# Optimization experiments

Measured on AMD Instinct MI355X. Metric: run time of the kernel, lower is better.

## Reference

```python
import jax, jax.numpy as jnp
import numpy as np

B, S, D, H = 2, 2048, 1024, 16
HD = D // H  # head_dim = 64
SCALE = HD ** -0.5


def setup_inputs() -> dict:
    key = jax.random.key(0)
    ks = jax.random.split(key, 10)
    std = D ** -0.5
    return {
        "x": jax.random.normal(ks[0], (B, S, D), jnp.float32),
        "y": jax.random.normal(ks[1], (B, S, D), jnp.float32),
        "Wq": jax.random.normal(ks[2], (D, D), jnp.float32) * std,
        "bq": jnp.zeros((D,), jnp.float32),
        "Wk": jax.random.normal(ks[3], (D, D), jnp.float32) * std,
        "bk": jnp.zeros((D,), jnp.float32),
        "Wv": jax.random.normal(ks[4], (D, D), jnp.float32) * std,
        "bv": jnp.zeros((D,), jnp.float32),
        "Wo": jax.random.normal(ks[5], (D, D), jnp.float32) * std,
        "bo": jnp.zeros((D,), jnp.float32),
    }


def reference(x, y, Wq, bq, Wk, bk, Wv, bv, Wo, bo):
    # Linear projections (torch Linear: x @ W.T + b; here W stored as [in,out])
    q = x @ Wq + bq  # [B,S,D]
    k = y @ Wk + bk
    v = y @ Wv + bv
    # split heads -> [B,H,S,hd]
    q = q.reshape(B, S, H, HD).transpose(0, 2, 1, 3)
    k = k.reshape(B, S, H, HD).transpose(0, 2, 1, 3)
    v = v.reshape(B, S, H, HD).transpose(0, 2, 1, 3)
    scores = jnp.einsum("bhqd,bhkd->bhqk", q, k) * SCALE  # [B,H,S,S]
    causal = jnp.tril(jnp.ones((S, S), dtype=bool))  # keep lower triangle
    scores = jnp.where(causal[None, None], scores, -jnp.inf)
    attn = jax.nn.softmax(scores, axis=-1)
    out = jnp.einsum("bhqk,bhkd->bhqd", attn, v)  # [B,H,S,hd]
    out = out.transpose(0, 2, 1, 3).reshape(B, S, D)
    return out @ Wo + bo
```

## Files before the change

### kernel.cpp

```cpp
#include <hip/hip_runtime.h>
#include <hip/hip_bf16.h>


#define BDIM 2
#define SDIM 2048
#define DDIM 1024
#define HDIM 16
#define HD   64
#define MDIM (BDIM*SDIM)
#define C2 0.18033688011112042f

using short8  = __attribute__((ext_vector_type(8))) short;
using floatx4 = __attribute__((ext_vector_type(4))) float;

static __device__ __forceinline__ unsigned short f2bf(float x) {
    union { float f; unsigned int u; } c; c.f = x;
    unsigned int r = (c.u + 0x7fffu + ((c.u >> 16) & 1u)) >> 16;
    return (unsigned short)r;
}

static __device__ __forceinline__ unsigned int pack2bf(float a, float b) {
    union { float f; unsigned int u; } ua, ub;
    ua.f = a; ub.f = b;
    return __builtin_amdgcn_perm(ub.u + 0x8000u, ua.u + 0x8000u, 0x07060302u);
}

#define GLD16(g, l) __builtin_amdgcn_global_load_lds(                        \
    (const __attribute__((address_space(1))) void*)(g),                      \
    (__attribute__((address_space(3))) void*)(l), 16, 0, 0)

__global__ __launch_bounds__(256) void prep_kernel(
    const float* __restrict__ X, const float* __restrict__ Y,
    const float* __restrict__ W0, const float* __restrict__ W1,
    const float* __restrict__ W2, const float* __restrict__ W3,
    unsigned short* __restrict__ Xo, unsigned short* __restrict__ Yo,
    unsigned short* __restrict__ T0, unsigned short* __restrict__ T1,
    unsigned short* __restrict__ T2, unsigned short* __restrict__ T3)
{
    __shared__ float tile[64][68];
    const int z = blockIdx.z;
    const int t = threadIdx.x;
    if (z < 2) {
        const float* A    = z ? Y : X;
        unsigned short* O = z ? Yo : Xo;
        const int idx = blockIdx.x * 256 + t;
        const float4 a = ((const float4*)A)[idx*2];
        const float4 b = ((const float4*)A)[idx*2 + 1];
        ushort4 lo, hi;
        lo.x = f2bf(a.x); lo.y = f2bf(a.y); lo.z = f2bf(a.z); lo.w = f2bf(a.w);
        hi.x = f2bf(b.x); hi.y = f2bf(b.y); hi.z = f2bf(b.z); hi.w = f2bf(b.w);
        ((ushort4*)O)[idx*2]     = lo;
        ((ushort4*)O)[idx*2 + 1] = hi;
        return;
    }
    if (blockIdx.x >= 256) return;
    const int zz = z - 2;
    const float* W    = (zz == 0) ? W0 : (zz == 1) ? W1 : (zz == 2) ? W2 : W3;
    unsigned short* T = (zz == 0) ? T0 : (zz == 1) ? T1 : (zz == 2) ? T2 : T3;
    const int k0 = (blockIdx.x & 15) * 64, n0 = (blockIdx.x >> 4) * 64;
    #pragma unroll
    for (int i = 0; i < 4; ++i) {
        const int idx = t + i*256;
        const int kr = idx >> 4, c4 = idx & 15;
        float4 v = *(const float4*)&W[(size_t)(k0 + kr) * DDIM + n0 + c4*4];
        tile[kr][c4*4+0] = v.x; tile[kr][c4*4+1] = v.y;
        tile[kr][c4*4+2] = v.z; tile[kr][c4*4+3] = v.w;
    }
    __syncthreads();
    #pragma unroll
    for (int i = 0; i < 4; ++i) {
        const int idx = t + i*256;
        const int nr = idx >> 4, kc = idx & 15;
        ushort4 o;
        o.x = f2bf(tile[kc*4+0][nr]); o.y = f2bf(tile[kc*4+1][nr]);
        o.z = f2bf(tile[kc*4+2][nr]); o.w = f2bf(tile[kc*4+3][nr]);
        *(ushort4*)&T[(size_t)(n0 + nr) * DDIM + k0 + kc*4] = o;
    }
}

template <bool SWAP>
__device__ __forceinline__ void gemm128_core(
    const unsigned short* __restrict__ A, const unsigned short* __restrict__ Bt,
    int bm, int bn, unsigned short* As, unsigned short* Bs, floatx4 acc[4][4])
{
    const int t = threadIdx.x;
    const int w = t >> 6, l = t & 63;
    const int quad = l >> 4, col = l & 15;
    const int wr = (w >> 1) * 64, wc = (w & 1) * 64;

    const int c1 = t + 256;
    const int r0 = t >> 2,  o0 = (t & 3) * 8;
    const int r1 = c1 >> 2, o1 = (c1 & 3) * 8;

    const unsigned short* Ar0 = A  + (size_t)(bm + r0) * DDIM + o0;
    const unsigned short* Ar1 = A  + (size_t)(bm + r1) * DDIM + o1;
    const unsigned short* Br0 = Bt + (size_t)(bn + r0) * DDIM + o0;
    const unsigned short* Br1 = Bt + (size_t)(bn + r1) * DDIM + o1;

    GLD16(Ar0, As + t*8);
    GLD16(Ar1, As + c1*8);
    GLD16(Br0, Bs + t*8);
    GLD16(Br1, Bs + c1*8);

    for (int kt = 0; kt < DDIM; kt += 32) {
        const int cur = (kt >> 5) & 1;
        unsigned short* Asn = As + (cur ^ 1) * 4096;
        unsigned short* Bsn = Bs + (cur ^ 1) * 4096;
        __syncthreads();
        if (kt + 32 < DDIM) {
            GLD16(Ar0 + kt + 32, Asn + t*8);
            GLD16(Ar1 + kt + 32, Asn + c1*8);
            GLD16(Br0 + kt + 32, Bsn + t*8);
            GLD16(Br1 + kt + 32, Bsn + c1*8);
        }
        const unsigned short* Asc = As + cur*4096;
        const unsigned short* Bsc = Bs + cur*4096;
        short8 af[4], bfr[4];
        #pragma unroll
        for (int i = 0; i < 4; ++i)
            af[i] = *(const short8*)&Asc[(wr + i*16 + col)*32 + quad*8];
        #pragma unroll
        for (int j = 0; j < 4; ++j)
            bfr[j] = *(const short8*)&Bsc[(wc + j*16 + col)*32 + quad*8];
        #pragma unroll
        for (int i = 0; i < 4; ++i)
            #pragma unroll
            for (int j = 0; j < 4; ++j)
                acc[i][j] = SWAP
                    ? __builtin_amdgcn_mfma_f32_16x16x32_bf16(bfr[j], af[i], acc[i][j], 0, 0, 0)
                    : __builtin_amdgcn_mfma_f32_16x16x32_bf16(af[i], bfr[j], acc[i][j], 0, 0, 0);
    }
}

__global__ __launch_bounds__(256) void qkv_gemm_kernel(
    const unsigned short* __restrict__ xbf, const unsigned short* __restrict__ ybf,
    const unsigned short* __restrict__ Wqt, const unsigned short* __restrict__ Wkt,
    const unsigned short* __restrict__ Wvt,
    const float* __restrict__ bq, const float* __restrict__ bk,
    const float* __restrict__ bv,
    unsigned short* __restrict__ Qbf, unsigned short* __restrict__ Kbf,
    unsigned short* __restrict__ vT)
{
    __shared__ __align__(16) unsigned short As[2*4096];
    __shared__ __align__(16) unsigned short Bs[2*4096];

    const int z = blockIdx.z;
    const unsigned short* A  = (z == 0) ? xbf : ybf;
    const unsigned short* Wt = (z == 0) ? Wqt : (z == 1) ? Wkt : Wvt;
    const float* bp          = (z == 0) ? bq  : (z == 1) ? bk  : bv;

    const int bm = (blockIdx.x * 4 + (blockIdx.y & 3)) * 128;
    const int bn = (blockIdx.y >> 2) * 128;

    const int t = threadIdx.x;
    const int w = t >> 6, l = t & 63;
    const int quad = l >> 4, col = l & 15;
    const int wr = (w >> 1) * 64, wc = (w & 1) * 64;

    floatx4 acc[4][4] = {};

    if (z < 2) {
        gemm128_core<true>(A, Wt, bm, bn, As, Bs, acc);
        unsigned short* O = (z == 0) ? Qbf : Kbf;
        const float sc = (z == 0) ? C2 : 1.0f;
        float4 bias4[4];
        #pragma unroll
        for (int j = 0; j < 4; ++j)
            bias4[j] = *(const float4*)&bp[bn + wc + j*16 + quad*4];
        #pragma unroll
        for (int i = 0; i < 4; ++i) {
            const int m = bm + wr + i*16 + col;
            unsigned short* rowp = O + (size_t)m * DDIM;
            #pragma unroll
            for (int j = 0; j < 4; ++j) {
                const float v0 = (acc[i][j][0] + bias4[j].x) * sc;
                const float v1 = (acc[i][j][1] + bias4[j].y) * sc;
                const float v2 = (acc[i][j][2] + bias4[j].z) * sc;
                const float v3 = (acc[i][j][3] + bias4[j].w) * sc;
                uint2 pk;
                pk.x = pack2bf(v0, v1);
                pk.y = pack2bf(v2, v3);
                *(uint2*)&rowp[bn + wc + j*16 + quad*4] = pk;
            }
        }
    } else {
        gemm128_core<false>(A, Wt, bm, bn, As, Bs, acc);
        #pragma unroll
        for (int j = 0; j < 4; ++j) {
            const int gn = bn + wc + j*16 + col;
            const float bias = bp[gn];
            #pragma unroll
            for (int i = 0; i < 4; ++i) {
                const int gm0 = bm + wr + i*16 + quad*4;
                uint2 pk;
                pk.x = pack2bf(acc[i][j][0] + bias, acc[i][j][1] + bias);
                pk.y = pack2bf(acc[i][j][2] + bias, acc[i][j][3] + bias);
                *(uint2*)&vT[((size_t)((gm0 >> 11) * DDIM + gn)) * SDIM + (gm0 & 2047)] = pk;
            }
        }
    }
}

__global__ __launch_bounds__(256) void out_gemm_kernel(
    const unsigned short* __restrict__ Obf, const unsigned short* __restrict__ Wot,
    const float* __restrict__ bo, float* __restrict__ out)
{
    __shared__ __align__(16) unsigned short As[2*4096];
    __shared__ __align__(16) unsigned short Bs[2*2048];

    const int t = threadIdx.x;
    const int w = t >> 6, l = t & 63;
    const int quad = l >> 4, col = l & 15;

    const int j  = (blockIdx.x >> 3) + 2 * blockIdx.y;
    const int bm = ((blockIdx.x & 7) * 4 + (j & 3)) * 128;
    const int bn = (j >> 2) * 64;

    const int wr = (w >> 1) * 64, wc = (w & 1) * 32;

    const int r0 = t >> 2, o0 = (t & 3) * 8;
    const unsigned short* Ar0 = Obf + (size_t)(bm + r0) * DDIM + o0;
    const unsigned short* Ar1 = Obf + (size_t)(bm + 64 + r0) * DDIM + o0;
    const unsigned short* Br  = Wot + (size_t)(bn + r0) * DDIM + o0;

    floatx4 acc[4][2] = {};

    GLD16(Ar0, As + t*8);
    GLD16(Ar1, As + (t + 256)*8);
    GLD16(Br,  Bs + t*8);

    for (int kt = 0; kt < DDIM; kt += 32) {
        const int cur = (kt >> 5) & 1;
        unsigned short* Asn = As + (cur ^ 1) * 4096;
        unsigned short* Bsn = Bs + (cur ^ 1) * 2048;
        __syncthreads();
        if (kt + 32 < DDIM) {
            GLD16(Ar0 + kt + 32, Asn + t*8);
            GLD16(Ar1 + kt + 32, Asn + (t + 256)*8);
            GLD16(Br  + kt + 32, Bsn + t*8);
        }
        const unsigned short* Asc = As + cur*4096;
        const unsigned short* Bsc = Bs + cur*2048;
        short8 af[4], bfr[2];
        #pragma unroll
        for (int i = 0; i < 4; ++i)
            af[i] = *(const short8*)&Asc[(wr + i*16 + col)*32 + quad*8];
        #pragma unroll
        for (int j2 = 0; j2 < 2; ++j2)
            bfr[j2] = *(const short8*)&Bsc[(wc + j2*16 + col)*32 + quad*8];
        #pragma unroll
        for (int i = 0; i < 4; ++i)
            #pragma unroll
            for (int j2 = 0; j2 < 2; ++j2)
                acc[i][j2] = __builtin_amdgcn_mfma_f32_16x16x32_bf16(
                    bfr[j2], af[i], acc[i][j2], 0, 0, 0);
    }

    float4 bias4[2];
    #pragma unroll
    for (int j2 = 0; j2 < 2; ++j2)
        bias4[j2] = *(const float4*)&bo[bn + wc + j2*16 + quad*4];
    #pragma unroll
    for (int i = 0; i < 4; ++i) {
        const int m = bm + wr + i*16 + col;
        float* rowp = out + (size_t)m * DDIM;
        #pragma unroll
        for (int j2 = 0; j2 < 2; ++j2) {
            float4 o;
            o.x = acc[i][j2][0] + bias4[j2].x;
            o.y = acc[i][j2][1] + bias4[j2].y;
            o.z = acc[i][j2][2] + bias4[j2].z;
            o.w = acc[i][j2][3] + bias4[j2].w;
            *(float4*)&rowp[bn + wc + j2*16 + quad*4] = o;
        }
    }
}

__global__ __launch_bounds__(256, 2) void attn_mfma_kernel(
    const unsigned short* __restrict__ Qbf, const unsigned short* __restrict__ Kbf,
    const unsigned short* __restrict__ vT, unsigned short* __restrict__ Obf)
{
    __shared__ float ls[2][4*64];
    __shared__ __align__(16) floatx4 os[2][1024];

    const int t = threadIdx.x;
    const int w = t >> 6, l = t & 63;
    const int quad = l >> 4, col = l & 15;

    const int lin = blockIdx.x;
    const int jj  = lin >> 3, rem = jj & 3;
    const int p   = jj >> 2;
    const int b   = rem & 1;
    const int h   = (lin & 7) + 8 * (rem >> 1);

    const size_t hoff = (size_t)h * HD;
    const size_t bS   = (size_t)b * SDIM;
    const size_t bD   = (size_t)b * DDIM;

    const int rowp = ((col >> 2) << 3) | (col & 3);
    const unsigned short* kb0 = Kbf + bS * DDIM + hoff + quad*8;
    const unsigned short* vb0 = vT + (bD + hoff + col) * SDIM + quad*8;

    #pragma unroll 1
    for (int ph = 0; ph < 2; ++ph) {
        const int qT = ph ? p : (31 - p);
        const int qb = qT * 64;

        short8 qf[4][2];
        #pragma unroll
        for (int m = 0; m < 4; ++m)
            #pragma unroll
            for (int hf = 0; hf < 2; ++hf)
                qf[m][hf] = *(const short8*)
                    &Qbf[(bS + qb + m*16 + col) * DDIM + hoff + hf*32 + quad*8];

        floatx4 o[4][4] = {};
        float lrun[4] = {0.f, 0.f, 0.f, 0.f};

        #pragma unroll 1
        for (int it = w; it <= qT; it += 4) {
            const int ktb = it * 64;
            const bool diag = (it == qT);

            short8 kf[2][2][2];
            #pragma unroll
            for (int c = 0; c < 2; ++c)
                #pragma unroll
                for (int tt = 0; tt < 2; ++tt) {
                    const size_t row = (size_t)(ktb + c*32 + tt*4 + rowp);
                    kf[c][tt][0] = *(const short8*)&kb0[row * DDIM];
                    kf[c][tt][1] = *(const short8*)&kb0[row * DDIM + 32];
                }
            short8 vf[4][2];
            #pragma unroll
            for (int n = 0; n < 4; ++n)
                #pragma unroll
                for (int c = 0; c < 2; ++c)
                    vf[n][c] = *(const short8*)
                        &vb0[(size_t)(n*16) * SDIM + ktb + c*32];

            #pragma unroll
            for (int m = 0; m < 4; ++m) {
                #pragma unroll
                for (int c = 0; c < 2; ++c) {
                    if (diag && (c*32 > m*16 + 15)) continue;
                    const bool needm = diag && (c*32 + 31 > m*16);

                    floatx4 s0 = {}, s1 = {};
                    __builtin_amdgcn_s_setprio(1);
                    s0 = __builtin_amdgcn_mfma_f32_16x16x32_bf16(kf[c][0][0], qf[m][0], s0, 0, 0, 0);
                    s0 = __builtin_amdgcn_mfma_f32_16x16x32_bf16(kf[c][0][1], qf[m][1], s0, 0, 0, 0);
                    s1 = __builtin_amdgcn_mfma_f32_16x16x32_bf16(kf[c][1][0], qf[m][0], s1, 0, 0, 0);
                    s1 = __builtin_amdgcn_mfma_f32_16x16x32_bf16(kf[c][1][1], qf[m][1], s1, 0, 0, 0);
                    __builtin_amdgcn_s_setprio(0);

                    float p0[4], p1[4];
                    const int qrow = m*16 + col;
                    const int kls  = c*32 + quad*8;
                    #pragma unroll
                    for (int rr = 0; rr < 4; ++rr) {
                        p0[rr] = (needm && (kls + rr     > qrow)) ? 0.0f : exp2f(s0[rr]);
                        p1[rr] = (needm && (kls + 4 + rr > qrow)) ? 0.0f : exp2f(s1[rr]);
                    }
                    lrun[m] += ((p0[0]+p0[1]) + (p0[2]+p0[3]))
                             + ((p1[0]+p1[1]) + (p1[2]+p1[3]));

                    union { short8 v; unsigned int u[4]; } pf;
                    pf.u[0] = pack2bf(p0[0], p0[1]);
                    pf.u[1] = pack2bf(p0[2], p0[3]);
                    pf.u[2] = pack2bf(p1[0], p1[1]);
                    pf.u[3] = pack2bf(p1[2], p1[3]);

                    __builtin_amdgcn_s_setprio(1);
                    #pragma unroll
                    for (int n = 0; n < 4; ++n)
                        o[n][m] = __builtin_amdgcn_mfma_f32_16x16x32_bf16(
                            vf[n][c], pf.v, o[n][m], 0, 0, 0);
                    __builtin_amdgcn_s_setprio(0);
                }
            }
        }

        if (w >= 2) {
            const int s = w - 2;
            #pragma unroll
            for (int n = 0; n < 4; ++n)
                #pragma unroll
                for (int m = 0; m < 4; ++m)
                    os[s][(n*4 + m)*64 + l] = o[n][m];
            #pragma unroll
            for (int m = 0; m < 4; ++m)
                ls[s][m*64 + l] = lrun[m];
        }
        __syncthreads();
        if (w < 2) {
            #pragma unroll
            for (int n = 0; n < 4; ++n)
                #pragma unroll
                for (int m = 0; m < 4; ++m)
                    o[n][m] += os[w][(n*4 + m)*64 + l];
            #pragma unroll
            for (int m = 0; m < 4; ++m)
                lrun[m] += ls[w][m*64 + l];
        }
        __syncthreads();
        if (w == 1) {
            #pragma unroll
            for (int n = 0; n < 4; ++n)
                #pragma unroll
                for (int m = 0; m < 4; ++m)
                    os[0][(n*4 + m)*64 + l] = o[n][m];
            #pragma unroll
            for (int m = 0; m < 4; ++m)
                ls[0][m*64 + l] = lrun[m];
        }
        __syncthreads();
        if (w == 0) {
            #pragma unroll
            for (int m = 0; m < 4; ++m) {
                float lt = lrun[m] + ls[0][m*64 + l];
                lt += __shfl_xor(lt, 16);
                lt += __shfl_xor(lt, 32);
                const float inv = 1.0f / lt;
                #pragma unroll
                for (int n = 0; n < 4; ++n) {
                    const floatx4 ov = o[n][m] + os[0][(n*4 + m)*64 + l];
                    uint2 pk;
                    pk.x = pack2bf(ov[0] * inv, ov[1] * inv);
                    pk.y = pack2bf(ov[2] * inv, ov[3] * inv);
                    *(uint2*)&Obf[(bS + qb + m*16 + col) * DDIM
                                  + hoff + n*16 + quad*4] = pk;
                }
            }
        }
        __syncthreads();
    }
}

extern "C" void kernel_launch(void* const* d_in, const int* in_sizes, int n_in,
                              void* d_out, int out_size, void* d_ws, size_t ws_size,
                              hipStream_t stream) {
    const float* x  = (const float*)d_in[0];
    const float* y  = (const float*)d_in[1];
    const float* Wq = (const float*)d_in[2];
    const float* bq = (const float*)d_in[3];
    const float* Wk = (const float*)d_in[4];
    const float* bk = (const float*)d_in[5];
    const float* Wv = (const float*)d_in[6];
    const float* bv = (const float*)d_in[7];
    const float* Wo = (const float*)d_in[8];
    const float* bo = (const float*)d_in[9];
    float* out = (float*)d_out;

    const size_t mat  = (size_t)MDIM * DDIM;
    const size_t wmat = (size_t)DDIM * DDIM;
    unsigned short* p = (unsigned short*)d_ws;
    unsigned short* xbf = p;            p += mat;
    unsigned short* ybf = p;            p += mat;
    unsigned short* Wqt = p;            p += wmat;
    unsigned short* Wkt = p;            p += wmat;
    unsigned short* Wvt = p;            p += wmat;
    unsigned short* Wot = p;            p += wmat;
    unsigned short* Qbf = p;            p += mat;
    unsigned short* Kbf = p;            p += mat;
    unsigned short* vT  = p;            p += mat;
    unsigned short* Obf = p;            p += mat;

    hipLaunchKernelGGL(prep_kernel, dim3(MDIM*DDIM/8/256, 1, 6), dim3(256),
                       0, stream, x, y, Wq, Wk, Wv, Wo,
                       xbf, ybf, Wqt, Wkt, Wvt, Wot);

    hipLaunchKernelGGL(qkv_gemm_kernel, dim3(DDIM/128, MDIM/128, 3), dim3(256),
                       0, stream, xbf, ybf, Wqt, Wkt, Wvt, bq, bk, bv,
                       Qbf, Kbf, vT);

    hipLaunchKernelGGL(attn_mfma_kernel, dim3(512), dim3(256),
                       0, stream, Qbf, Kbf, vT, Obf);

    hipLaunchKernelGGL(out_gemm_kernel, dim3(DDIM/64, MDIM/128), dim3(256),
                       0, stream, Obf, Wot, bo, out);
}
```

Measured before the change: 207.8 us.

## Split attention query tiles in half to double grid and raise occupancy

Each attention block now handles 32 query rows instead of 64, and the grid doubles to 1024 blocks. Per-thread accumulators, Q fragments and shared reduction buffers shrink by half, and launch bounds go from 2 to 4 blocks per SIMD. The K/V loads now happen inside the per-chunk loop, and diagonal chunks beyond the half are skipped. The intent is more waves in flight and better load balance, at the cost of loading each K/V tile twice (once per half), which doubles K/V traffic.

```diff
diff --git a/kernel.cpp b/kernel.cpp
--- a/kernel.cpp
+++ b/kernel.cpp
@@ -276,22 +276,25 @@
     }
 }
 
-__global__ __launch_bounds__(256, 2) void attn_mfma_kernel(
+__global__ __launch_bounds__(256, 4) void attn_mfma_kernel(
     const unsigned short* __restrict__ Qbf, const unsigned short* __restrict__ Kbf,
     const unsigned short* __restrict__ vT, unsigned short* __restrict__ Obf)
 {
-    __shared__ float ls[2][4*64];
-    __shared__ __align__(16) floatx4 os[2][1024];
+    __shared__ float ls[2][2*64];
+    __shared__ __align__(16) floatx4 os[2][512];
 
     const int t = threadIdx.x;
     const int w = t >> 6, l = t & 63;
     const int quad = l >> 4, col = l & 15;
 
-    const int lin = blockIdx.x;
-    const int jj  = lin >> 3, rem = jj & 3;
-    const int p   = jj >> 2;
-    const int b   = rem & 1;
-    const int h   = (lin & 7) + 8 * (rem >> 1);
+    const int lin  = blockIdx.x;
+    const int j    = lin >> 3;
+    const int p    = j >> 3;
+    const int low  = j & 7;
+    const int b    = low & 1;
+    const int hh   = (low >> 1) & 1;
+    const int half = (low >> 2) & 1;
+    const int h    = (lin & 7) + 8 * hh;
 
     const size_t hoff = (size_t)h * HD;
     const size_t bS   = (size_t)b * SDIM;
@@ -303,59 +306,57 @@
 
     #pragma unroll 1
     for (int ph = 0; ph < 2; ++ph) {
-        const int qT = ph ? p : (31 - p);
-        const int qb = qT * 64;
-
-        short8 qf[4][2];
-        #pragma unroll
-        for (int m = 0; m < 4; ++m)
+        const int qT  = ph ? p : (31 - p);
+        const int qb2 = qT * 64 + half * 32;
+
+        short8 qf[2][2];
+        #pragma unroll
+        for (int m = 0; m < 2; ++m)
             #pragma unroll
             for (int hf = 0; hf < 2; ++hf)
                 qf[m][hf] = *(const short8*)
-                    &Qbf[(bS + qb + m*16 + col) * DDIM + hoff + hf*32 + quad*8];
-
-        floatx4 o[4][4] = {};
-        float lrun[4] = {0.f, 0.f, 0.f, 0.f};
+                    &Qbf[(bS + qb2 + m*16 + col) * DDIM + hoff + hf*32 + quad*8];
+
+        floatx4 o[4][2] = {};
+        float lrun[2] = {0.f, 0.f};
 
         #pragma unroll 1
         for (int it = w; it <= qT; it += 4) {
             const int ktb = it * 64;
             const bool diag = (it == qT);
 
-            short8 kf[2][2][2];
-            #pragma unroll
-            for (int c = 0; c < 2; ++c)
+            #pragma unroll
+            for (int c = 0; c < 2; ++c) {
+                if (diag && (c*32 > half*32 + 31)) continue;
+
+                short8 kfc[2][2];
                 #pragma unroll
                 for (int tt = 0; tt < 2; ++tt) {
                     const size_t row = (size_t)(ktb + c*32 + tt*4 + rowp);
-                    kf[c][tt][0] = *(const short8*)&kb0[row * DDIM];
-                    kf[c][tt][1] = *(const short8*)&kb0[row * DDIM + 32];
+                    kfc[tt][0] = *(const short8*)&kb0[row * DDIM];
+                    kfc[tt][1] = *(const short8*)&kb0[row * DDIM + 32];
                 }
-            short8 vf[4][2];
-            #pragma unroll
-            for (int n = 0; n < 4; ++n)
-                #pragma unroll
-                for (int c = 0; c < 2; ++c)
-                    vf[n][c] = *(const short8*)
+                short8 vfc[4];
+                #pragma unroll
+                for (int n = 0; n < 4; ++n)
+                    vfc[n] = *(const short8*)
                         &vb0[(size_t)(n*16) * SDIM + ktb + c*32];
 
-            #pragma unroll
-            for (int m = 0; m < 4; ++m) {
-                #pragma unroll
-                for (int c = 0; c < 2; ++c) {
-                    if (diag && (c*32 > m*16 + 15)) continue;
-                    const bool needm = diag && (c*32 + 31 > m*16);
+                #pragma unroll
+                for (int m = 0; m < 2; ++m) {
+                    const int mrow = half*32 + m*16;
+                    const bool needm = diag && (c*32 + 31 > mrow);
 
                     floatx4 s0 = {}, s1 = {};
                     __builtin_amdgcn_s_setprio(1);
-                    s0 = __builtin_amdgcn_mfma_f32_16x16x32_bf16(kf[c][0][0], qf[m][0], s0, 0, 0, 0);
-                    s0 = __builtin_amdgcn_mfma_f32_16x16x32_bf16(kf[c][0][1], qf[m][1], s0, 0, 0, 0);
-                    s1 = __builtin_amdgcn_mfma_f32_16x16x32_bf16(kf[c][1][0], qf[m][0], s1, 0, 0, 0);
-                    s1 = __builtin_amdgcn_mfma_f32_16x16x32_bf16(kf[c][1][1], qf[m][1], s1, 0, 0, 0);
+                    s0 = __builtin_amdgcn_mfma_f32_16x16x32_bf16(kfc[0][0], qf[m][0], s0, 0, 0, 0);
+                    s0 = __builtin_amdgcn_mfma_f32_16x16x32_bf16(kfc[0][1], qf[m][1], s0, 0, 0, 0);
+                    s1 = __builtin_amdgcn_mfma_f32_16x16x32_bf16(kfc[1][0], qf[m][0], s1, 0, 0, 0);
+                    s1 = __builtin_amdgcn_mfma_f32_16x16x32_bf16(kfc[1][1], qf[m][1], s1, 0, 0, 0);
                     __builtin_amdgcn_s_setprio(0);
 
                     float p0[4], p1[4];
-                    const int qrow = m*16 + col;
+                    const int qrow = mrow + col;
                     const int kls  = c*32 + quad*8;
                     #pragma unroll
                     for (int rr = 0; rr < 4; ++rr) {
@@ -375,7 +376,7 @@
                     #pragma unroll
                     for (int n = 0; n < 4; ++n)
                         o[n][m] = __builtin_amdgcn_mfma_f32_16x16x32_bf16(
-                            vf[n][c], pf.v, o[n][m], 0, 0, 0);
+                            vfc[n], pf.v, o[n][m], 0, 0, 0);
                     __builtin_amdgcn_s_setprio(0);
                 }
             }
@@ -386,10 +387,10 @@
             #pragma unroll
             for (int n = 0; n < 4; ++n)
                 #pragma unroll
-                for (int m = 0; m < 4; ++m)
-                    os[s][(n*4 + m)*64 + l] = o[n][m];
-            #pragma unroll
-            for (int m = 0; m < 4; ++m)
+                for (int m = 0; m < 2; ++m)
+                    os[s][(n*2 + m)*64 + l] = o[n][m];
+            #pragma unroll
+            for (int m = 0; m < 2; ++m)
                 ls[s][m*64 + l] = lrun[m];
         }
         __syncthreads();
@@ -397,10 +398,10 @@
             #pragma unroll
             for (int n = 0; n < 4; ++n)
                 #pragma unroll
-                for (int m = 0; m < 4; ++m)
-                    o[n][m] += os[w][(n*4 + m)*64 + l];
-            #pragma unroll
-            for (int m = 0; m < 4; ++m)
+                for (int m = 0; m < 2; ++m)
+                    o[n][m] += os[w][(n*2 + m)*64 + l];
+            #pragma unroll
+            for (int m = 0; m < 2; ++m)
                 lrun[m] += ls[w][m*64 + l];
         }
         __syncthreads();
@@ -408,27 +409,27 @@
             #pragma unroll
             for (int n = 0; n < 4; ++n)
                 #pragma unroll
-                for (int m = 0; m < 4; ++m)
-                    os[0][(n*4 + m)*64 + l] = o[n][m];
-            #pragma unroll
-            for (int m = 0; m < 4; ++m)
+                for (int m = 0; m < 2; ++m)
+                    os[0][(n*2 + m)*64 + l] = o[n][m];
+            #pragma unroll
+            for (int m = 0; m < 2; ++m)
                 ls[0][m*64 + l] = lrun[m];
         }
         __syncthreads();
         if (w == 0) {
             #pragma unroll
-            for (int m = 0; m < 4; ++m) {
+            for (int m = 0; m < 2; ++m) {
                 float lt = lrun[m] + ls[0][m*64 + l];
                 lt += __shfl_xor(lt, 16);
                 lt += __shfl_xor(lt, 32);
                 const float inv = 1.0f / lt;
                 #pragma unroll
                 for (int n = 0; n < 4; ++n) {
-                    const floatx4 ov = o[n][m] + os[0][(n*4 + m)*64 + l];
+                    const floatx4 ov = o[n][m] + os[0][(n*2 + m)*64 + l];
                     uint2 pk;
                     pk.x = pack2bf(ov[0] * inv, ov[1] * inv);
                     pk.y = pack2bf(ov[2] * inv, ov[3] * inv);
-                    *(uint2*)&Obf[(bS + qb + m*16 + col) * DDIM
+                    *(uint2*)&Obf[(bS + qb2 + m*16 + col) * DDIM
                                   + hoff + n*16 + quad*4] = pk;
                 }
             }
@@ -474,7 +475,7 @@
                        0, stream, xbf, ybf, Wqt, Wkt, Wvt, bq, bk, bv,
                        Qbf, Kbf, vT);
 
-    hipLaunchKernelGGL(attn_mfma_kernel, dim3(512), dim3(256),
+    hipLaunchKernelGGL(attn_mfma_kernel, dim3(1024), dim3(256),
                        0, stream, Qbf, Kbf, vT, Obf);
 
     hipLaunchKernelGGL(out_gemm_kernel, dim3(DDIM/64, MDIM/128), dim3(256),
```

New measurement: 230.3 us. 1.11x slower.

## Double-buffer K tiles in LDS via async global-to-LDS loads in attention

Applied to the files above, without the earlier changes.

The attention kernel now stages each wave's 64-row K tile into a per-wave double-buffered LDS slot using direct global-to-LDS loads (GLD16), prefetching the next tile while computing the current one. K fragments are then read from LDS instead of from scattered global rows. The reduction scratch arrays are aliased onto the same 64KB shared buffer, and a barrier is added before they are reused. This raises LDS use to 64KB per block, which may limit occupancy under launch_bounds(256,2), and relies on hand-written vmcnt waits being correct.

```diff
diff --git a/kernel.cpp b/kernel.cpp
--- a/kernel.cpp
+++ b/kernel.cpp
@@ -280,8 +280,9 @@
     const unsigned short* __restrict__ Qbf, const unsigned short* __restrict__ Kbf,
     const unsigned short* __restrict__ vT, unsigned short* __restrict__ Obf)
 {
-    __shared__ float ls[2][4*64];
-    __shared__ __align__(16) floatx4 os[2][1024];
+    __shared__ __align__(16) unsigned short SH[32768];
+    floatx4* os = (floatx4*)SH;
+    float*   ls = (float*)(SH + 16384);
 
     const int t = threadIdx.x;
     const int w = t >> 6, l = t & 63;
@@ -298,8 +299,18 @@
     const size_t bD   = (size_t)b * DDIM;
 
     const int rowp = ((col >> 2) << 3) | (col & 3);
-    const unsigned short* kb0 = Kbf + bS * DDIM + hoff + quad*8;
     const unsigned short* vb0 = vT + (bD + hoff + col) * SDIM + quad*8;
+    const unsigned short* kst = Kbf + (bS + (l >> 3)) * DDIM + hoff + (l & 7)*8;
+    unsigned short* slot0 = &SH[(w * 2) * 4096];
+
+#define STAGEK(BUFI, ITV)                                                    \
+    do {                                                                     \
+        unsigned short* dst_ = slot0 + (BUFI) * 4096;                        \
+        const unsigned short* src_ = kst + (size_t)(ITV) * 64 * DDIM;        \
+        _Pragma("unroll")                                                    \
+        for (int js_ = 0; js_ < 8; ++js_)                                    \
+            GLD16(src_ + (size_t)js_ * 8 * DDIM, dst_ + js_ * 512);          \
+    } while (0)
 
     #pragma unroll 1
     for (int ph = 0; ph < 2; ++ph) {
@@ -317,20 +328,14 @@
         floatx4 o[4][4] = {};
         float lrun[4] = {0.f, 0.f, 0.f, 0.f};
 
+        int cur = 0;
+        if (w <= qT) STAGEK(0, w);
+
         #pragma unroll 1
         for (int it = w; it <= qT; it += 4) {
             const int ktb = it * 64;
             const bool diag = (it == qT);
 
-            short8 kf[2][2][2];
-            #pragma unroll
-            for (int c = 0; c < 2; ++c)
-                #pragma unroll
-                for (int tt = 0; tt < 2; ++tt) {
-                    const size_t row = (size_t)(ktb + c*32 + tt*4 + rowp);
-                    kf[c][tt][0] = *(const short8*)&kb0[row * DDIM];
-                    kf[c][tt][1] = *(const short8*)&kb0[row * DDIM + 32];
-                }
             short8 vf[4][2];
             #pragma unroll
             for (int n = 0; n < 4; ++n)
@@ -338,6 +343,25 @@
                 for (int c = 0; c < 2; ++c)
                     vf[n][c] = *(const short8*)
                         &vb0[(size_t)(n*16) * SDIM + ktb + c*32];
+
+            if (it + 4 <= qT) {
+                STAGEK(cur ^ 1, it + 4);
+                asm volatile("s_waitcnt vmcnt(16)" ::: "memory");
+            } else {
+                asm volatile("s_waitcnt vmcnt(8)" ::: "memory");
+            }
+            __builtin_amdgcn_sched_barrier(0);
+
+            const unsigned short* kslot = slot0 + cur * 4096;
+            short8 kf[2][2][2];
+            #pragma unroll
+            for (int c = 0; c < 2; ++c)
+                #pragma unroll
+                for (int tt = 0; tt < 2; ++tt) {
+                    const int r = c*32 + tt*4 + rowp;
+                    kf[c][tt][0] = *(const short8*)&kslot[r*64 + quad*8];
+                    kf[c][tt][1] = *(const short8*)&kslot[r*64 + 32 + quad*8];
+                }
 
             #pragma unroll
             for (int m = 0; m < 4; ++m) {
@@ -379,7 +403,10 @@
                     __builtin_amdgcn_s_setprio(0);
                 }
             }
-        }
+            cur ^= 1;
+        }
+
+        __syncthreads();
 
         if (w >= 2) {
             const int s = w - 2;
@@ -387,10 +414,10 @@
             for (int n = 0; n < 4; ++n)
                 #pragma unroll
                 for (int m = 0; m < 4; ++m)
-                    os[s][(n*4 + m)*64 + l] = o[n][m];
+                    os[s*1024 + (n*4 + m)*64 + l] = o[n][m];
             #pragma unroll
             for (int m = 0; m < 4; ++m)
-                ls[s][m*64 + l] = lrun[m];
+                ls[s*256 + m*64 + l] = lrun[m];
         }
         __syncthreads();
         if (w < 2) {
@@ -398,10 +425,10 @@
             for (int n = 0; n < 4; ++n)
                 #pragma unroll
                 for (int m = 0; m < 4; ++m)
-                    o[n][m] += os[w][(n*4 + m)*64 + l];
+                    o[n][m] += os[w*1024 + (n*4 + m)*64 + l];
             #pragma unroll
             for (int m = 0; m < 4; ++m)
-                lrun[m] += ls[w][m*64 + l];
+                lrun[m] += ls[w*256 + m*64 + l];
         }
         __syncthreads();
         if (w == 1) {
@@ -409,22 +436,22 @@
             for (int n = 0; n < 4; ++n)
                 #pragma unroll
                 for (int m = 0; m < 4; ++m)
-                    os[0][(n*4 + m)*64 + l] = o[n][m];
+                    os[(n*4 + m)*64 + l] = o[n][m];
             #pragma unroll
             for (int m = 0; m < 4; ++m)
-                ls[0][m*64 + l] = lrun[m];
+                ls[m*64 + l] = lrun[m];
         }
         __syncthreads();
         if (w == 0) {
             #pragma unroll
             for (int m = 0; m < 4; ++m) {
-                float lt = lrun[m] + ls[0][m*64 + l];
+                float lt = lrun[m] + ls[m*64 + l];
                 lt += __shfl_xor(lt, 16);
                 lt += __shfl_xor(lt, 32);
                 const float inv = 1.0f / lt;
                 #pragma unroll
                 for (int n = 0; n < 4; ++n) {
-                    const floatx4 ov = o[n][m] + os[0][(n*4 + m)*64 + l];
+                    const floatx4 ov = o[n][m] + os[(n*4 + m)*64 + l];
                     uint2 pk;
                     pk.x = pack2bf(ov[0] * inv, ov[1] * inv);
                     pk.y = pack2bf(ov[2] * inv, ov[3] * inv);
@@ -435,6 +462,7 @@
         }
         __syncthreads();
     }
+#undef STAGEK
 }
 
 extern "C" void kernel_launch(void* const* d_in, const int* in_sizes, int n_in,
```

Result: no change. 207.2 us (-0.3%).

## Split attention query tile across two wave groups with 512-thread blocks

Applied to the files above, without the earlier changes.

Doubles the attention block to 8 waves: each group of 4 waves handles 32 of the 64 query rows, while the key tiles are still strided across 4 waves. This halves the per-wave accumulator and Q fragment registers, which raises occupancy and wave count per CU. In exchange, K and V fragments are loaded twice per block (once by each row group), and the reduction through shared memory now runs per half.

```diff
diff --git a/kernel.cpp b/kernel.cpp
--- a/kernel.cpp
+++ b/kernel.cpp
@@ -276,15 +276,16 @@
     }
 }
 
-__global__ __launch_bounds__(256, 2) void attn_mfma_kernel(
+__global__ __launch_bounds__(512, 4) void attn_mfma_kernel(
     const unsigned short* __restrict__ Qbf, const unsigned short* __restrict__ Kbf,
     const unsigned short* __restrict__ vT, unsigned short* __restrict__ Obf)
 {
-    __shared__ float ls[2][4*64];
-    __shared__ __align__(16) floatx4 os[2][1024];
+    __shared__ __align__(16) floatx4 os[2][2][512];
+    __shared__ float ls[2][2][128];
 
     const int t = threadIdx.x;
     const int w = t >> 6, l = t & 63;
+    const int kw = w & 3, mh = w >> 2;
     const int quad = l >> 4, col = l & 15;
 
     const int lin = blockIdx.x;
@@ -306,19 +307,20 @@
         const int qT = ph ? p : (31 - p);
         const int qb = qT * 64;
 
-        short8 qf[4][2];
-        #pragma unroll
-        for (int m = 0; m < 4; ++m)
+        short8 qf[2][2];
+        #pragma unroll
+        for (int m = 0; m < 2; ++m)
             #pragma unroll
             for (int hf = 0; hf < 2; ++hf)
                 qf[m][hf] = *(const short8*)
-                    &Qbf[(bS + qb + m*16 + col) * DDIM + hoff + hf*32 + quad*8];
-
-        floatx4 o[4][4] = {};
-        float lrun[4] = {0.f, 0.f, 0.f, 0.f};
+                    &Qbf[(bS + qb + mh*32 + m*16 + col) * DDIM
+                         + hoff + hf*32 + quad*8];
+
+        floatx4 o[4][2] = {};
+        float lrun[2] = {0.f, 0.f};
 
         #pragma unroll 1
-        for (int it = w; it <= qT; it += 4) {
+        for (int it = kw; it <= qT; it += 4) {
             const int ktb = it * 64;
             const bool diag = (it == qT);
 
@@ -340,11 +342,12 @@
                         &vb0[(size_t)(n*16) * SDIM + ktb + c*32];
 
             #pragma unroll
-            for (int m = 0; m < 4; ++m) {
+            for (int m = 0; m < 2; ++m) {
+                const int mrow = mh*32 + m*16;
                 #pragma unroll
                 for (int c = 0; c < 2; ++c) {
-                    if (diag && (c*32 > m*16 + 15)) continue;
-                    const bool needm = diag && (c*32 + 31 > m*16);
+                    if (diag && (c*32 > mrow + 15)) continue;
+                    const bool needm = diag && (c*32 + 31 > mrow);
 
                     floatx4 s0 = {}, s1 = {};
                     __builtin_amdgcn_s_setprio(1);
@@ -355,7 +358,7 @@
                     __builtin_amdgcn_s_setprio(0);
 
                     float p0[4], p1[4];
-                    const int qrow = m*16 + col;
+                    const int qrow = mrow + col;
                     const int kls  = c*32 + quad*8;
                     #pragma unroll
                     for (int rr = 0; rr < 4; ++rr) {
@@ -381,54 +384,54 @@
             }
         }
 
-        if (w >= 2) {
-            const int s = w - 2;
+        if (kw >= 2) {
+            const int s = kw - 2;
             #pragma unroll
             for (int n = 0; n < 4; ++n)
                 #pragma unroll
-                for (int m = 0; m < 4; ++m)
-                    os[s][(n*4 + m)*64 + l] = o[n][m];
-            #pragma unroll
-            for (int m = 0; m < 4; ++m)
-                ls[s][m*64 + l] = lrun[m];
-        }
-        __syncthreads();
-        if (w < 2) {
+                for (int m = 0; m < 2; ++m)
+                    os[mh][s][(n*2 + m)*64 + l] = o[n][m];
+            #pragma unroll
+            for (int m = 0; m < 2; ++m)
+                ls[mh][s][m*64 + l] = lrun[m];
+        }
+        __syncthreads();
+        if (kw < 2) {
             #pragma unroll
             for (int n = 0; n < 4; ++n)
                 #pragma unroll
-                for (int m = 0; m < 4; ++m)
-                    o[n][m] += os[w][(n*4 + m)*64 + l];
-            #pragma unroll
-            for (int m = 0; m < 4; ++m)
-                lrun[m] += ls[w][m*64 + l];
-        }
-        __syncthreads();
-        if (w == 1) {
+                for (int m = 0; m < 2; ++m)
+                    o[n][m] += os[mh][kw][(n*2 + m)*64 + l];
+            #pragma unroll
+            for (int m = 0; m < 2; ++m)
+                lrun[m] += ls[mh][kw][m*64 + l];
+        }
+        __syncthreads();
+        if (kw == 1) {
             #pragma unroll
             for (int n = 0; n < 4; ++n)
                 #pragma unroll
-                for (int m = 0; m < 4; ++m)
-                    os[0][(n*4 + m)*64 + l] = o[n][m];
-            #pragma unroll
-            for (int m = 0; m < 4; ++m)
-                ls[0][m*64 + l] = lrun[m];
-        }
-        __syncthreads();
-        if (w == 0) {
-            #pragma unroll
-            for (int m = 0; m < 4; ++m) {
-                float lt = lrun[m] + ls[0][m*64 + l];
+                for (int m = 0; m < 2; ++m)
+                    os[mh][0][(n*2 + m)*64 + l] = o[n][m];
+            #pragma unroll
+            for (int m = 0; m < 2; ++m)
+                ls[mh][0][m*64 + l] = lrun[m];
+        }
+        __syncthreads();
+        if (kw == 0) {
+            #pragma unroll
+            for (int m = 0; m < 2; ++m) {
+                float lt = lrun[m] + ls[mh][0][m*64 + l];
                 lt += __shfl_xor(lt, 16);
                 lt += __shfl_xor(lt, 32);
                 const float inv = 1.0f / lt;
                 #pragma unroll
                 for (int n = 0; n < 4; ++n) {
-                    const floatx4 ov = o[n][m] + os[0][(n*4 + m)*64 + l];
+                    const floatx4 ov = o[n][m] + os[mh][0][(n*2 + m)*64 + l];
                     uint2 pk;
                     pk.x = pack2bf(ov[0] * inv, ov[1] * inv);
                     pk.y = pack2bf(ov[2] * inv, ov[3] * inv);
-                    *(uint2*)&Obf[(bS + qb + m*16 + col) * DDIM
+                    *(uint2*)&Obf[(bS + qb + mh*32 + m*16 + col) * DDIM
                                   + hoff + n*16 + quad*4] = pk;
                 }
             }
@@ -474,7 +477,7 @@
                        0, stream, xbf, ybf, Wqt, Wkt, Wvt, bq, bk, bv,
                        Qbf, Kbf, vT);
 
-    hipLaunchKernelGGL(attn_mfma_kernel, dim3(512), dim3(256),
+    hipLaunchKernelGGL(attn_mfma_kernel, dim3(512), dim3(512),
                        0, stream, Qbf, Kbf, vT, Obf);
 
     hipLaunchKernelGGL(out_gemm_kernel, dim3(DDIM/64, MDIM/128), dim3(256),
```

Measured after the change: 259.2 us. 24.7% more time.
